# Performance work log

Hardware: AMD Instinct MI355X
Metric: run time of the kernel (lower is better)

The kernel has to match this reference:

```python
import jax, jax.numpy as jnp
import numpy as np
import math

N, E = 50000, 800000
DM, H, L = 128, 8, 6
D = DM // H  # per-head dim = 16
FF = 4 * DM
EPS = 1e-5


def _ln(x, g, b):
    mu = jnp.mean(x, axis=-1, keepdims=True)
    var = jnp.mean((x - mu) ** 2, axis=-1, keepdims=True)
    return (x - mu) * jax.lax.rsqrt(var + EPS) * g + b


def setup_inputs() -> dict:
    key = jax.random.key(0)
    ks = jax.random.split(key, 20)
    s = 0.05
    inp = {
        "node_features": jax.random.normal(ks[0], (N, 20), jnp.float32),
        "edge_attr": jax.random.normal(ks[1], (E, 3), jnp.float32),
        "edge_index": jax.random.randint(ks[2], (2, E), 0, N, jnp.int32),
        "emb_W": jax.random.normal(ks[3], (20, DM), jnp.float32) * s,
        "emb_b": jnp.zeros((DM,), jnp.float32),
        "Wq": jax.random.normal(ks[4], (L, DM, DM), jnp.float32) * s,
        "Wk": jax.random.normal(ks[5], (L, DM, DM), jnp.float32) * s,
        "Wv": jax.random.normal(ks[6], (L, DM, DM), jnp.float32) * s,
        "eW1": jax.random.normal(ks[7], (L, 3, D), jnp.float32) * s,
        "eb1": jnp.zeros((L, D), jnp.float32),
        "eW2": jax.random.normal(ks[8], (L, D, DM), jnp.float32) * s,
        "eb2": jnp.zeros((L, DM), jnp.float32),
        "ln_g": jnp.ones((L, DM), jnp.float32),
        "ln_b": jnp.zeros((L, DM), jnp.float32),
        "ff_W1": jax.random.normal(ks[9], (L, DM, FF), jnp.float32) * s,
        "ff_b1": jnp.zeros((L, FF), jnp.float32),
        "ff_W2": jax.random.normal(ks[10], (L, FF, DM), jnp.float32) * s,
        "ff_b2": jnp.zeros((L, DM), jnp.float32),
    }
    return inp


def reference(node_features, edge_attr, emb_W, emb_b, Wq, Wk, Wv,
              eW1, eb1, eW2, eb2, ln_g, ln_b, ff_W1, ff_b1, ff_W2, ff_b2,
              edge_index):
    src = edge_index[0]  # j: message source
    dst = edge_index[1]  # i: message target
    x = node_features @ emb_W + emb_b  # [N, DM]
    scale = 1.0 / math.sqrt(D)
    for l in range(L):
        q = (x @ Wq[l]).reshape(N, H, D)
        k = (x @ Wk[l]).reshape(N, H, D)
        v = (x @ Wv[l]).reshape(N, H, D)
        ee = (jnp.maximum(edge_attr @ eW1[l] + eb1[l], 0.0) @ eW2[l] + eb2[l]).reshape(E, H, D)
        # per-edge attention logits over heads (softmax over head axis, as in source)
        attn = jnp.einsum('ehd,ehd->eh', q[dst], k[src] + ee) * scale
        attn = jax.nn.softmax(attn, axis=1)  # [E, H]
        msg = (attn[..., None] * v[src]).reshape(E, H * D)  # per-head messages, concat heads
        agg = jax.ops.segment_sum(msg, dst, num_segments=N)  # scatter-add
        x = _ln(x + agg, ln_g[l], ln_b[l])
        h = jnp.maximum(x @ ff_W1[l] + ff_b1[l], 0.0) @ ff_W2[l] + ff_b2[l]
        x = _ln(x + h, ln_g[l], ln_b[l])  # same LN params reused, as in source
    return x
```

## Files before the change

### kernel.cpp

```cpp
#include <hip/hip_runtime.h>
#include <cstdint>
#include <cstddef>

#define NN 50000
#define NE 800000
#define NP 50048
#define ROWT 391
#define NBLK 196

typedef unsigned short u16;
typedef _Float16 f16;
typedef _Float16 hf8 __attribute__((ext_vector_type(8)));
typedef float f32x4 __attribute__((ext_vector_type(4)));

union U32 { unsigned u; f16 h[2]; };
union U64 { uint2 v; f16 h[4]; };
union U128 { uint4 v; f16 x[8]; };

__device__ __forceinline__ float b2f(u16 v){ return __uint_as_float((unsigned)v << 16); }
__device__ __forceinline__ u16 f2b(float f){
  unsigned u = __float_as_uint(f);
  return (u16)((u + 0x7fffu + ((u >> 16) & 1u)) >> 16);
}
__device__ __forceinline__ float ldf(const void* p, long i, int f32){
  return f32 ? ((const float*)p)[i] : b2f(((const u16*)p)[i]);
}
__device__ __forceinline__ void gl_lds16(const void* g, void* l){
  __builtin_amdgcn_global_load_lds((const __attribute__((address_space(1))) void*)g,
                                   (__attribute__((address_space(3))) void*)l, 16, 0, 0);
}

__global__ void detect_k(const u16* __restrict__ nf, int* __restrict__ flag)
{
  int mx = 0;
  for (int i = 0; i < 256; ++i) { int e = (nf[i] >> 7) & 0xFF; mx = e > mx ? e : mx; }
  flag[0] = (mx >= 0x90) ? 1 : 0;
}

__global__ void zero_i_k(int* __restrict__ p, int n)
{
  int i = blockIdx.x * 256 + threadIdx.x;
  if (i < n) p[i] = 0;
}

__global__ void conv_k(const void* eW1, const void* eb1, const void* eb2,
                       const void* lng, const void* lnb, const void* fb1, const void* fb2,
                       const void* embB, const void* embW,
                       float* __restrict__ pf, const int* __restrict__ dflag)
{
  int f32 = dflag[0];
  int i = blockIdx.x * 256 + threadIdx.x;
  if (i >= 9216) return;
  const void* p; long off;
  if (i < 288)       { p = eW1;  off = i; }
  else if (i < 384)  { p = eb1;  off = i - 288; }
  else if (i < 1152) { p = eb2;  off = i - 384; }
  else if (i < 1920) { p = lng;  off = i - 1152; }
  else if (i < 2688) { p = lnb;  off = i - 1920; }
  else if (i < 5760) { p = fb1;  off = i - 2688; }
  else if (i < 6528) { p = fb2;  off = i - 5760; }
  else if (i < 6656) { p = embB; off = i - 6528; }
  else               { p = embW; off = i - 6656; }
  pf[i] = ldf(p, off, f32);
}

__global__ void prep_qkve_k(const void* __restrict__ Wq, const void* __restrict__ Wk,
                            const void* __restrict__ Wv, const void* __restrict__ eW2,
                            f16* __restrict__ Wcat, const int* __restrict__ dflag)
{
  int f32 = dflag[0];
  int idx = blockIdx.x * 256 + threadIdx.x;
  int l = idx >> 16;
  int rem = idx & 65535;
  int r = rem >> 7;
  int kk = rem & 127;
  long base = (long)l * 16384;
  float val;
  if (r < 384) {
    const void* W = (r < 128) ? Wq : (r < 256) ? Wk : Wv;
    int n = r & 127;
    val = ldf(W, base + kk * 128 + n, f32);
  } else {
    int n = r - 384, h = n >> 4, j = n & 15;
    long wq = base + kk * 128 + h * 16;
    long e2 = (long)l * 2048 + j * 128 + h * 16;
    float s = 0.f;
    #pragma unroll
    for (int d = 0; d < 16; ++d) s += ldf(Wq, wq + d, f32) * ldf(eW2, e2 + d, f32);
    val = s;
  }
  Wcat[idx] = (f16)val;
}

__global__ void transpose_k(const void* __restrict__ in, f16* __restrict__ out, int R, int C,
                            const int* __restrict__ dflag)
{
  int f32 = dflag[0];
  int idx = blockIdx.x * 256 + threadIdx.x;
  int rc = R * C;
  int l = idx / rc, rem = idx % rc;
  int r = rem / C, c = rem % C;
  out[l * rc + c * R + r] = (f16)ldf(in, idx, f32);
}

__global__ void deg_count_k(const int* __restrict__ eidx, int* __restrict__ deg)
{
  int e = blockIdx.x * 256 + threadIdx.x;
  if (e < NE) atomicAdd(&deg[eidx[NE + e]], 1);
}

__global__ void scan_a(const int* __restrict__ deg, int* __restrict__ bsum)
{
  __shared__ int tmp[256];
  int t = threadIdx.x, i = blockIdx.x * 256 + t;
  int v = (i < NN) ? deg[i] : 0;
  tmp[t] = v; __syncthreads();
  for (int o = 1; o < 256; o <<= 1) {
    int u = (t >= o) ? tmp[t - o] : 0;
    __syncthreads(); tmp[t] += u; __syncthreads();
  }
  if (t == 255) bsum[blockIdx.x] = tmp[255];
}

__global__ void scan_b(const int* __restrict__ bsum, int* __restrict__ boff)
{
  __shared__ int tmp[256];
  int t = threadIdx.x;
  int v = (t < NBLK) ? bsum[t] : 0;
  tmp[t] = v; __syncthreads();
  for (int o = 1; o < 256; o <<= 1) {
    int u = (t >= o) ? tmp[t - o] : 0;
    __syncthreads(); tmp[t] += u; __syncthreads();
  }
  if (t < NBLK) boff[t] = tmp[t] - v;
}

__global__ void scan_c(const int* __restrict__ deg, const int* __restrict__ boff,
                       int* __restrict__ rstart, int* __restrict__ cursor)
{
  __shared__ int tmp[256];
  int t = threadIdx.x, i = blockIdx.x * 256 + t;
  int v = (i < NN) ? deg[i] : 0;
  tmp[t] = v; __syncthreads();
  for (int o = 1; o < 256; o <<= 1) {
    int u = (t >= o) ? tmp[t - o] : 0;
    __syncthreads(); tmp[t] += u; __syncthreads();
  }
  if (i <= NN) {
    int ex = boff[blockIdx.x] + tmp[t] - v;
    rstart[i] = ex;
    if (i < NN) cursor[i] = ex;
  }
}

__global__ void csr_fill_k(const int* __restrict__ eidx, int* __restrict__ cursor,
                           int* __restrict__ csrc, int* __restrict__ ceid)
{
  int e = blockIdx.x * 256 + threadIdx.x;
  if (e >= NE) return;
  int d = eidx[NE + e];
  int slot = atomicAdd(&cursor[d], 1);
  csrc[slot] = eidx[e];
  ceid[slot] = e;
}

__global__ void ea_gather_k(const void* __restrict__ eatt, const int* __restrict__ ceid,
                            f16* __restrict__ ea4, const int* __restrict__ dflag)
{
  int f32 = dflag[0];
  int e = blockIdx.x * 256 + threadIdx.x;
  if (e >= NE) return;
  long id = ceid[e];
  f16* q = ea4 + (size_t)e * 4;
  q[0] = (f16)ldf(eatt, id * 3 + 0, f32);
  q[1] = (f16)ldf(eatt, id * 3 + 1, f32);
  q[2] = (f16)ldf(eatt, id * 3 + 2, f32);
  q[3] = (f16)0.f;
}

__global__ void emb_k(const void* __restrict__ nf, const float* __restrict__ embWf,
                      const float* __restrict__ embBf, float* __restrict__ xf,
                      f16* __restrict__ xh, const int* __restrict__ dflag)
{
  int f32 = dflag[0];
  int idx = blockIdx.x * 256 + threadIdx.x;
  int node = idx >> 7, c = idx & 127;
  float s = 0.f;
  if (node < NN) {
    s = embBf[c];
    long row = (long)node * 20;
    #pragma unroll
    for (int f = 0; f < 20; ++f) s += ldf(nf, row + f, f32) * embWf[f * 128 + c];
  }
  xf[idx] = s;
  xh[idx] = (f16)s;
}

template<int MODE>
__global__ __launch_bounds__(256)
void gemm_k(const f16* __restrict__ A, const f16* __restrict__ Bt, int K,
            f16* __restrict__ o0, f16* __restrict__ o1, f16* __restrict__ o3,
            const float* __restrict__ bias,
            const float* __restrict__ gf, const float* __restrict__ bpf,
            float* __restrict__ xf, f16* __restrict__ xh)
{
  __shared__ __align__(16) f16 sh[128 * 256];
  f16* lA = sh;
  f16* lB = sh + 16384;
  const int tid = threadIdx.x;
  const int wave = tid >> 6, lane = tid & 63;
  const int wr = wave >> 1, wc = wave & 1;
  const size_t rowBase = (size_t)blockIdx.x * 128;
  const size_t colBase = (size_t)blockIdx.y * 128;
  const int m = lane & 15, q4 = lane >> 4;

  f32x4 zero = {0.f, 0.f, 0.f, 0.f};
  f32x4 acc[4][4];
  #pragma unroll
  for (int i = 0; i < 4; ++i)
    #pragma unroll
    for (int j = 0; j < 4; ++j) acc[i][j] = zero;

  const int sr4 = lane >> 4, sc16 = lane & 15;
  const f16* Ap = A + (rowBase + wave * 32 + sr4) * (size_t)K + sc16 * 8;
  const f16* Bp = Bt + (colBase + wave * 32 + sr4) * (size_t)K + sc16 * 8;
  f16* lAp = lA + wave * 4096;
  f16* lBp = lB + wave * 4096;

  for (int k0 = 0; k0 < K; k0 += 128) {
    #pragma unroll
    for (int i = 0; i < 8; ++i) {
      gl_lds16(Ap + k0 + (size_t)(4 * i) * K, lAp + i * 512);
      gl_lds16(Bp + k0 + (size_t)(4 * i) * K, lBp + i * 512);
    }
    __syncthreads();
    #pragma unroll
    for (int kk = 0; kk < 4; ++kk) {
      hf8 af[4], bf[4];
      #pragma unroll
      for (int i = 0; i < 4; ++i) {
        af[i] = *(const hf8*)(lA + (wr * 64 + i * 16 + m) * 128 + kk * 32 + q4 * 8);
        bf[i] = *(const hf8*)(lB + (wc * 64 + i * 16 + m) * 128 + kk * 32 + q4 * 8);
      }
      #pragma unroll
      for (int i = 0; i < 4; ++i)
        #pragma unroll
        for (int j = 0; j < 4; ++j)
          acc[i][j] = __builtin_amdgcn_mfma_f32_16x16x32_f16(bf[j], af[i], acc[i][j], 0, 0, 0);
    }
    __syncthreads();
  }

  #pragma unroll
  for (int i = 0; i < 4; ++i) {
    int crow = wr * 64 + i * 16 + m;
    #pragma unroll
    for (int j = 0; j < 4; ++j) {
      int ccol = wc * 64 + j * 16 + q4 * 4;
      float v[4];
      #pragma unroll
      for (int r = 0; r < 4; ++r) v[r] = acc[i][j][r];
      if (MODE == 1) {
        float4 bv = *(const float4*)(bias + (int)colBase + ccol);
        v[0] = fmaxf(v[0] + bv.x, 0.f); v[1] = fmaxf(v[1] + bv.y, 0.f);
        v[2] = fmaxf(v[2] + bv.z, 0.f); v[3] = fmaxf(v[3] + bv.w, 0.f);
      } else if (MODE == 2) {
        float4 bv = *(const float4*)(bias + ccol);
        v[0] += bv.x; v[1] += bv.y; v[2] += bv.z; v[3] += bv.w;
      }
      U64 pk;
      #pragma unroll
      for (int r = 0; r < 4; ++r) pk.h[r] = (f16)v[r];
      *(uint2*)(sh + crow * 136 + ccol) = pk.v;
    }
  }
  __syncthreads();

  if (MODE != 2) {
    f16* o; size_t ld; int off;
    if (MODE == 0) {
      if (blockIdx.y == 0)      { o = o0; ld = 128; off = 0; }
      else if (blockIdx.y == 1) { o = o1; ld = 256; off = 0; }
      else if (blockIdx.y == 2) { o = o1; ld = 256; off = 128; }
      else                      { o = o3; ld = 128; off = 0; }
    } else { o = o0; ld = 512; off = (int)colBase; }
    int row = tid >> 1, half = tid & 1;
    const f16* srcp = sh + row * 136 + half * 64;
    f16* dstp = o + (rowBase + row) * ld + off + half * 64;
    #pragma unroll
    for (int k = 0; k < 8; ++k)
      *(uint4*)(dstp + k * 8) = *(const uint4*)(srcp + k * 8);
  } else {
    int row = tid >> 1, half = tid & 1;
    size_t nb = (rowBase + row) * (size_t)128 + half * 64;
    const f16* srcp = sh + row * 136 + half * 64;
    float y[64];
    float s1 = 0.f, s2 = 0.f;
    #pragma unroll
    for (int k = 0; k < 8; ++k) {
      U128 u; u.v = *(const uint4*)(srcp + k * 8);
      float4 xa = *(const float4*)(xf + nb + k * 8);
      float4 xb = *(const float4*)(xf + nb + k * 8 + 4);
      float xr[8] = { xa.x, xa.y, xa.z, xa.w, xb.x, xb.y, xb.z, xb.w };
      #pragma unroll
      for (int d = 0; d < 8; ++d) {
        float t = (float)u.x[d] + xr[d];
        y[k * 8 + d] = t; s1 += t; s2 += t * t;
      }
    }
    s1 += __shfl_xor(s1, 1); s2 += __shfl_xor(s2, 1);
    float mu = s1 * 0.0078125f;
    float var = s2 * 0.0078125f - mu * mu;
    float rstd = rsqrtf(var + 1e-5f);
    int cb = half * 64;
    #pragma unroll
    for (int k = 0; k < 8; ++k) {
      float4 oa, ob; U128 pk;
      #pragma unroll
      for (int d = 0; d < 4; ++d) {
        float ov = (y[k * 8 + d] - mu) * rstd * gf[cb + k * 8 + d] + bpf[cb + k * 8 + d];
        (&oa.x)[d] = ov; pk.x[d] = (f16)ov;
      }
      #pragma unroll
      for (int d = 0; d < 4; ++d) {
        float ov = (y[k * 8 + 4 + d] - mu) * rstd * gf[cb + k * 8 + 4 + d] + bpf[cb + k * 8 + 4 + d];
        (&ob.x)[d] = ov; pk.x[4 + d] = (f16)ov;
      }
      *(float4*)(xf + nb + k * 8) = oa;
      *(float4*)(xf + nb + k * 8 + 4) = ob;
      *(uint4*)(xh + nb + k * 8) = pk.v;
    }
  }
}

__global__ void fuse_k(const f16* __restrict__ qf, const f16* __restrict__ qef,
                       const f16* __restrict__ kv, const f16* __restrict__ ea4,
                       const int* __restrict__ rstart, const int* __restrict__ csrc,
                       const float* __restrict__ eW1f, const float* __restrict__ eb1f,
                       const float* __restrict__ eb2f,
                       const float* __restrict__ gf, const float* __restrict__ bpf,
                       float* __restrict__ xf, f16* __restrict__ xh)
{
  int wave = threadIdx.x >> 6, lane = threadIdx.x & 63;
  int node = blockIdx.x * 4 + wave;
  if (node >= NN) return;
  int sub = lane >> 4, l = lane & 15;
  int c0 = l << 3;
  int half = l & 1;
  size_t nb = (size_t)node * 128 + c0;

  float q[8], z[8];
  { U128 u; u.v = *(const uint4*)(qf + nb);
    #pragma unroll
    for (int i = 0; i < 8; ++i) q[i] = (float)u.x[i];
    u.v = *(const uint4*)(qef + nb);
    #pragma unroll
    for (int i = 0; i < 8; ++i) z[i] = (float)u.x[i]; }

  float pb = 0.f;
  #pragma unroll
  for (int i = 0; i < 8; ++i) pb = fmaf(q[i], eb2f[c0 + i], pb);
  pb += __shfl_xor(pb, 1);

  int j0 = half << 3;
  float w0[8], w1[8], w2[8], bb[8];
  #pragma unroll
  for (int i = 0; i < 8; ++i) {
    w0[i] = eW1f[j0 + i];
    w1[i] = eW1f[16 + j0 + i];
    w2[i] = eW1f[32 + j0 + i];
    bb[i] = eb1f[j0 + i];
  }

  float acc[8] = {0.f, 0.f, 0.f, 0.f, 0.f, 0.f, 0.f, 0.f};
  int e0 = rstart[node], e1 = rstart[node + 1];
  int e = e0 + sub;
  uint4 kN = {0,0,0,0}, vN = {0,0,0,0};
  uint2 eaN = {0,0};
  if (e < e1) {
    int s = csrc[e];
    const f16* kb = kv + (size_t)s * 256 + c0;
    kN = *(const uint4*)kb;
    vN = *(const uint4*)(kb + 128);
    eaN = *(const uint2*)(ea4 + (size_t)e * 4);
  }
  for (; e < e1; e += 4) {
    uint4 kC = kN, vC = vN; uint2 eaC = eaN;
    int en = e + 4;
    if (en < e1) {
      int s = csrc[en];
      const f16* kb = kv + (size_t)s * 256 + c0;
      kN = *(const uint4*)kb;
      vN = *(const uint4*)(kb + 128);
      eaN = *(const uint2*)(ea4 + (size_t)en * 4);
    }
    U64 ue; ue.v = eaC;
    float a0 = (float)ue.h[0], a1 = (float)ue.h[1], a2 = (float)ue.h[2];
    U128 K; K.v = kC;
    float p = 0.f;
    #pragma unroll
    for (int i = 0; i < 8; ++i) {
      float h = fmaxf(fmaf(a2, w2[i], fmaf(a1, w1[i], fmaf(a0, w0[i], bb[i]))), 0.f);
      p = fmaf(q[i], (float)K.x[i], fmaf(z[i], h, p));
    }
    p += __shfl_xor(p, 1);
    float logit = (p + pb) * 0.25f;
    float mx = logit;
    mx = fmaxf(mx, __shfl_xor(mx, 2));
    mx = fmaxf(mx, __shfl_xor(mx, 4));
    mx = fmaxf(mx, __shfl_xor(mx, 8));
    float ex = __expf(logit - mx);
    float se = ex;
    se += __shfl_xor(se, 2); se += __shfl_xor(se, 4); se += __shfl_xor(se, 8);
    float w = ex / se;
    U128 V; V.v = vC;
    #pragma unroll
    for (int i = 0; i < 8; ++i) acc[i] = fmaf(w, (float)V.x[i], acc[i]);
  }

  #pragma unroll
  for (int i = 0; i < 8; ++i) {
    acc[i] += __shfl_xor(acc[i], 16);
    acc[i] += __shfl_xor(acc[i], 32);
  }
  float4 x0 = *(const float4*)(xf + nb);
  float4 x1 = *(const float4*)(xf + nb + 4);
  float y[8] = { x0.x + acc[0], x0.y + acc[1], x0.z + acc[2], x0.w + acc[3],
                 x1.x + acc[4], x1.y + acc[5], x1.z + acc[6], x1.w + acc[7] };
  float s1 = 0.f, s2 = 0.f;
  #pragma unroll
  for (int i = 0; i < 8; ++i) { s1 += y[i]; s2 += y[i] * y[i]; }
  #pragma unroll
  for (int o = 1; o < 16; o <<= 1) { s1 += __shfl_xor(s1, o); s2 += __shfl_xor(s2, o); }
  float mu = s1 * 0.0078125f;
  float var = s2 * 0.0078125f - mu * mu;
  float rstd = rsqrtf(var + 1e-5f);
  float ov[8];
  #pragma unroll
  for (int i = 0; i < 8; ++i) ov[i] = (y[i] - mu) * rstd * gf[c0 + i] + bpf[c0 + i];
  if (sub == 0) {
    float4 s0 = { ov[0], ov[1], ov[2], ov[3] };
    float4 s1v = { ov[4], ov[5], ov[6], ov[7] };
    *(float4*)(xf + nb) = s0;
    *(float4*)(xf + nb + 4) = s1v;
    U128 wz;
    #pragma unroll
    for (int i = 0; i < 8; ++i) wz.x[i] = (f16)ov[i];
    *(uint4*)(xh + nb) = wz.v;
  }
}

__global__ void out_k(const float* __restrict__ xf, void* __restrict__ out,
                      const int* __restrict__ dflag)
{
  int f32 = dflag[0];
  int idx = blockIdx.x * 256 + threadIdx.x;
  if (f32) ((float*)out)[idx] = xf[idx];
  else     ((u16*)out)[idx] = f2b(xf[idx]);
}

extern "C" void kernel_launch(void* const* d_in, const int* in_sizes, int n_in,
                              void* d_out, int out_size, void* d_ws, size_t ws_size,
                              hipStream_t stream)
{
  const void* nf   = d_in[0];
  const void* eatt = d_in[1];
  const int*  eidx = (const int*)d_in[2];
  const void* embW = d_in[3];
  const void* embB = d_in[4];
  const void* Wq   = d_in[5];
  const void* Wk   = d_in[6];
  const void* Wv   = d_in[7];
  const void* eW1  = d_in[8];
  const void* eb1  = d_in[9];
  const void* eW2  = d_in[10];
  const void* eb2  = d_in[11];
  const void* lng  = d_in[12];
  const void* lnb  = d_in[13];
  const void* fW1  = d_in[14];
  const void* fb1  = d_in[15];
  const void* fW2  = d_in[16];
  const void* fb2  = d_in[17];

  char* p = (char*)d_ws;
  auto alloc = [&](size_t b) { char* r = p; p += (b + 255) & ~(size_t)255; return r; };
  int* dflag   = (int*)alloc(256);
  float* pf    = (float*)alloc(9216 * 4);
  float* xf    = (float*)alloc((size_t)NP * 128 * 4);
  f16*   xh    = (f16*)  alloc((size_t)NP * 128 * 2);
  int* deg     = (int*)alloc((NN + 1) * 4);
  int* rst     = (int*)alloc((NN + 1) * 4);
  int* cur     = (int*)alloc((size_t)NN * 4);
  int* bsum    = (int*)alloc(NBLK * 4);
  int* boff    = (int*)alloc(NBLK * 4);
  int* csrc    = (int*)alloc((size_t)NE * 4);
  f16* ea4     = (f16*)alloc((size_t)NE * 4 * 2);
  f16* Wcat    = (f16*)alloc((size_t)6 * 512 * 128 * 2);
  f16* W1t     = (f16*)alloc((size_t)6 * 512 * 128 * 2);
  f16* W2t     = (f16*)alloc((size_t)6 * 128 * 512 * 2);
  char* S    = alloc((size_t)NP * 512 * 2 + (size_t)NP * 128 * 2);
  f16* qf  = (f16*)S;
  f16* qe  = qf + (size_t)NP * 128;
  f16* kv  = qe + (size_t)NP * 128;
  f16* hb  = (f16*)S;
  int* ceid = (int*)S;

  float* eW1f = pf;
  float* eb1f = pf + 288;
  float* eb2f = pf + 384;
  float* lngf = pf + 1152;
  float* lnbf = pf + 1920;
  float* fb1f = pf + 2688;
  float* fb2f = pf + 5760;
  float* embBf = pf + 6528;
  float* embWf = pf + 6656;

  detect_k<<<1, 1, 0, stream>>>((const u16*)nf, dflag);
  conv_k<<<36, 256, 0, stream>>>(eW1, eb1, eb2, lng, lnb, fb1, fb2, embB, embW, pf, dflag);
  prep_qkve_k<<<1536, 256, 0, stream>>>(Wq, Wk, Wv, eW2, Wcat, dflag);
  transpose_k<<<1536, 256, 0, stream>>>(fW1, W1t, 128, 512, dflag);
  transpose_k<<<1536, 256, 0, stream>>>(fW2, W2t, 512, 128, dflag);
  zero_i_k<<<(NN + 256) / 256, 256, 0, stream>>>(deg, NN + 1);
  deg_count_k<<<3125, 256, 0, stream>>>(eidx, deg);
  scan_a<<<NBLK, 256, 0, stream>>>(deg, bsum);
  scan_b<<<1, 256, 0, stream>>>(bsum, boff);
  scan_c<<<NBLK, 256, 0, stream>>>(deg, boff, rst, cur);
  csr_fill_k<<<3125, 256, 0, stream>>>(eidx, cur, csrc, ceid);
  ea_gather_k<<<3125, 256, 0, stream>>>(eatt, ceid, ea4, dflag);
  emb_k<<<NP * 128 / 256, 256, 0, stream>>>(nf, embWf, embBf, xf, xh, dflag);

  for (int l = 0; l < 6; ++l) {
    gemm_k<0><<<dim3(ROWT, 4), 256, 0, stream>>>(xh, Wcat + (size_t)l * 65536, 128,
                                                 qf, kv, qe, nullptr,
                                                 nullptr, nullptr, nullptr, nullptr);
    fuse_k<<<12500, 256, 0, stream>>>(qf, qe, kv, ea4, rst, csrc,
                                      eW1f + l * 48, eb1f + l * 16, eb2f + l * 128,
                                      lngf + l * 128, lnbf + l * 128, xf, xh);
    gemm_k<1><<<dim3(ROWT, 4), 256, 0, stream>>>(xh, W1t + (size_t)l * 65536, 128,
                                                 hb, nullptr, nullptr, fb1f + l * 512,
                                                 nullptr, nullptr, nullptr, nullptr);
    gemm_k<2><<<dim3(ROWT, 1), 256, 0, stream>>>(hb, W2t + (size_t)l * 65536, 512,
                                                 nullptr, nullptr, nullptr, fb2f + l * 128,
                                                 lngf + l * 128, lnbf + l * 128, xf, xh);
  }
  out_k<<<25000, 256, 0, stream>>>(xf, d_out, dflag);
}
```

Before: 1.539 ms.

## Halve GEMM LDS tile to K=64 and write MODE 0/1 outputs directly from registers

The GEMM k-step drops from 128 to 64, which halves the shared-memory footprint (64KB to 32KB, or about 34KB for MODE 2). That should let more blocks fit on each CU and improve latency hiding. For MODE 0 and 1 the MFMA operand order is swapped so each lane holds a column, and results are stored straight to global memory as scalar f16 writes. This removes the LDS staging pass and one barrier. The cost is twice as many barriers per K, and the scalar 2-byte global stores may coalesce worse than the previous 16-byte row stores.

```diff
diff --git a/kernel.cpp b/kernel.cpp
--- a/kernel.cpp
+++ b/kernel.cpp
@@ -204,9 +204,9 @@
             const float* __restrict__ gf, const float* __restrict__ bpf,
             float* __restrict__ xf, f16* __restrict__ xh)
 {
-  __shared__ __align__(16) f16 sh[128 * 256];
+  __shared__ __align__(16) f16 sh[MODE == 2 ? 17408 : 16384];
   f16* lA = sh;
-  f16* lB = sh + 16384;
+  f16* lB = sh + 8192;
   const int tid = threadIdx.x;
   const int wave = tid >> 6, lane = tid & 63;
   const int wr = wave >> 1, wc = wave & 1;
@@ -221,76 +221,88 @@
     #pragma unroll
     for (int j = 0; j < 4; ++j) acc[i][j] = zero;
 
-  const int sr4 = lane >> 4, sc16 = lane & 15;
-  const f16* Ap = A + (rowBase + wave * 32 + sr4) * (size_t)K + sc16 * 8;
-  const f16* Bp = Bt + (colBase + wave * 32 + sr4) * (size_t)K + sc16 * 8;
-  f16* lAp = lA + wave * 4096;
-  f16* lBp = lB + wave * 4096;
-
-  for (int k0 = 0; k0 < K; k0 += 128) {
-    #pragma unroll
-    for (int i = 0; i < 8; ++i) {
-      gl_lds16(Ap + k0 + (size_t)(4 * i) * K, lAp + i * 512);
-      gl_lds16(Bp + k0 + (size_t)(4 * i) * K, lBp + i * 512);
+  const int sr = lane >> 3, sc = lane & 7;
+  const f16* Ap = A + (rowBase + wave * 32 + sr) * (size_t)K + sc * 8;
+  const f16* Bp = Bt + (colBase + wave * 32 + sr) * (size_t)K + sc * 8;
+  f16* lAp = lA + wave * 2048;
+  f16* lBp = lB + wave * 2048;
+
+  for (int k0 = 0; k0 < K; k0 += 64) {
+    #pragma unroll
+    for (int i = 0; i < 4; ++i) {
+      gl_lds16(Ap + k0 + (size_t)(8 * i) * K, lAp + i * 512);
+      gl_lds16(Bp + k0 + (size_t)(8 * i) * K, lBp + i * 512);
     }
     __syncthreads();
-    #pragma unroll
-    for (int kk = 0; kk < 4; ++kk) {
-      hf8 af[4], bf[4];
+    hf8 af[2][4], bf[2][4];
+    #pragma unroll
+    for (int s = 0; s < 2; ++s)
       #pragma unroll
       for (int i = 0; i < 4; ++i) {
-        af[i] = *(const hf8*)(lA + (wr * 64 + i * 16 + m) * 128 + kk * 32 + q4 * 8);
-        bf[i] = *(const hf8*)(lB + (wc * 64 + i * 16 + m) * 128 + kk * 32 + q4 * 8);
+        af[s][i] = *(const hf8*)(lA + (wr * 64 + i * 16 + m) * 64 + s * 32 + q4 * 8);
+        bf[s][i] = *(const hf8*)(lB + (wc * 64 + i * 16 + m) * 64 + s * 32 + q4 * 8);
       }
+    #pragma unroll
+    for (int s = 0; s < 2; ++s)
       #pragma unroll
       for (int i = 0; i < 4; ++i)
         #pragma unroll
-        for (int j = 0; j < 4; ++j)
-          acc[i][j] = __builtin_amdgcn_mfma_f32_16x16x32_f16(bf[j], af[i], acc[i][j], 0, 0, 0);
-    }
+        for (int j = 0; j < 4; ++j) {
+          if (MODE == 2)
+            acc[i][j] = __builtin_amdgcn_mfma_f32_16x16x32_f16(bf[s][j], af[s][i], acc[i][j], 0, 0, 0);
+          else
+            acc[i][j] = __builtin_amdgcn_mfma_f32_16x16x32_f16(af[s][i], bf[s][j], acc[i][j], 0, 0, 0);
+        }
     __syncthreads();
   }
 
-  #pragma unroll
-  for (int i = 0; i < 4; ++i) {
-    int crow = wr * 64 + i * 16 + m;
+  if (MODE == 0) {
+    f16* o; size_t ld; int off;
+    if (blockIdx.y == 0)      { o = o0; ld = 128; off = 0; }
+    else if (blockIdx.y == 1) { o = o1; ld = 256; off = 0; }
+    else if (blockIdx.y == 2) { o = o1; ld = 256; off = 128; }
+    else                      { o = o3; ld = 128; off = 0; }
+    #pragma unroll
+    for (int i = 0; i < 4; ++i)
+      #pragma unroll
+      for (int r = 0; r < 4; ++r) {
+        size_t row = rowBase + wr * 64 + i * 16 + q4 * 4 + r;
+        #pragma unroll
+        for (int j = 0; j < 4; ++j) {
+          int col = wc * 64 + j * 16 + m;
+          o[row * ld + off + col] = (f16)acc[i][j][r];
+        }
+      }
+  } else if (MODE == 1) {
     #pragma unroll
     for (int j = 0; j < 4; ++j) {
-      int ccol = wc * 64 + j * 16 + q4 * 4;
-      float v[4];
-      #pragma unroll
-      for (int r = 0; r < 4; ++r) v[r] = acc[i][j][r];
-      if (MODE == 1) {
-        float4 bv = *(const float4*)(bias + (int)colBase + ccol);
-        v[0] = fmaxf(v[0] + bv.x, 0.f); v[1] = fmaxf(v[1] + bv.y, 0.f);
-        v[2] = fmaxf(v[2] + bv.z, 0.f); v[3] = fmaxf(v[3] + bv.w, 0.f);
-      } else if (MODE == 2) {
+      int colg = (int)colBase + wc * 64 + j * 16 + m;
+      float bv = bias[colg];
+      #pragma unroll
+      for (int i = 0; i < 4; ++i)
+        #pragma unroll
+        for (int r = 0; r < 4; ++r) {
+          size_t row = rowBase + wr * 64 + i * 16 + q4 * 4 + r;
+          o0[row * 512 + colg] = (f16)fmaxf(acc[i][j][r] + bv, 0.f);
+        }
+    }
+  } else {
+    #pragma unroll
+    for (int i = 0; i < 4; ++i) {
+      int crow = wr * 64 + i * 16 + m;
+      #pragma unroll
+      for (int j = 0; j < 4; ++j) {
+        int ccol = wc * 64 + j * 16 + q4 * 4;
         float4 bv = *(const float4*)(bias + ccol);
-        v[0] += bv.x; v[1] += bv.y; v[2] += bv.z; v[3] += bv.w;
+        U64 pk;
+        pk.h[0] = (f16)(acc[i][j][0] + bv.x);
+        pk.h[1] = (f16)(acc[i][j][1] + bv.y);
+        pk.h[2] = (f16)(acc[i][j][2] + bv.z);
+        pk.h[3] = (f16)(acc[i][j][3] + bv.w);
+        *(uint2*)(sh + crow * 136 + ccol) = pk.v;
       }
-      U64 pk;
-      #pragma unroll
-      for (int r = 0; r < 4; ++r) pk.h[r] = (f16)v[r];
-      *(uint2*)(sh + crow * 136 + ccol) = pk.v;
-    }
-  }
-  __syncthreads();
-
-  if (MODE != 2) {
-    f16* o; size_t ld; int off;
-    if (MODE == 0) {
-      if (blockIdx.y == 0)      { o = o0; ld = 128; off = 0; }
-      else if (blockIdx.y == 1) { o = o1; ld = 256; off = 0; }
-      else if (blockIdx.y == 2) { o = o1; ld = 256; off = 128; }
-      else                      { o = o3; ld = 128; off = 0; }
-    } else { o = o0; ld = 512; off = (int)colBase; }
-    int row = tid >> 1, half = tid & 1;
-    const f16* srcp = sh + row * 136 + half * 64;
-    f16* dstp = o + (rowBase + row) * ld + off + half * 64;
-    #pragma unroll
-    for (int k = 0; k < 8; ++k)
-      *(uint4*)(dstp + k * 8) = *(const uint4*)(srcp + k * 8);
-  } else {
+    }
+    __syncthreads();
     int row = tid >> 1, half = tid & 1;
     size_t nb = (rowBase + row) * (size_t)128 + half * 64;
     const f16* srcp = sh + row * 136 + half * 64;
```

New measurement: 1.330 ms. 1.16x faster.
